# Kernel tuning notes

Hardware: AMD Instinct MI355X
Metric: run time of the kernel (lower is better)

The kernel has to match this reference:

```python
import jax, jax.numpy as jnp
import numpy as np

B, L = 8192, 2048  # L = 2*T, interleaved (dx, dy) increments


def setup_inputs() -> dict:
    key = jax.random.key(0)
    k1, k2, k3 = jax.random.split(key, 3)
    return {
        "traj_pred": jax.random.normal(k1, (B, L), dtype=jnp.float32),
        "traj_du_true": jax.random.normal(k2, (B, L), dtype=jnp.float32),  # unused in loss math
        "traj_pos_true": jax.random.normal(k3, (B, L), dtype=jnp.float32),
    }


def reference(traj_pred, traj_du_true, traj_pos_true):
    # pred[2k], pred[2k+1] are per-step (dx, dy) increments -> cumulative position
    T = traj_pred.shape[1] // 2
    d = traj_pred.reshape(traj_pred.shape[0], T, 2)  # [B, T, 2]
    pos = jnp.cumsum(d, axis=1)                      # [B, T, 2] running (x, y)
    tx = traj_pos_true[:, :T]                        # true x positions
    ty = traj_pos_true[:, T:]                        # true y positions
    err = (pos[..., 0] - tx) ** 2 + (pos[..., 1] - ty) ** 2
    return jnp.sum(err)
```

## Files before the change

### kernel.cpp

```cpp
#include <hip/hip_runtime.h>


constexpr int L_DIM = 2048;
constexpr int T_DIM = 1024;
constexpr int ROWS_PER_BLOCK = 4;
constexpr int NJ = 8;

__global__ __launch_bounds__(256, 4) void traj_loss_kernel(
    const float* __restrict__ pred,
    const float* __restrict__ pos_true,
    float* __restrict__ partials,
    int B)
{
    const int wid  = threadIdx.x >> 6;
    const int lane = threadIdx.x & 63;
    const int row  = blockIdx.x * ROWS_PER_BLOCK + wid;

    float acc = 0.0f;

    if (row < B) {
        const float4* p4  = reinterpret_cast<const float4*>(pred + (size_t)row * L_DIM);
        const float2* tX2 = reinterpret_cast<const float2*>(pos_true + (size_t)row * L_DIM);
        const float2* tY2 = reinterpret_cast<const float2*>(pos_true + (size_t)row * L_DIM + T_DIM);

        float4 v[NJ];
        float2 tx[NJ], ty[NJ];
#pragma unroll
        for (int j = 0; j < NJ; ++j) v[j]  = p4[j * 64 + lane];
#pragma unroll
        for (int j = 0; j < NJ; ++j) tx[j] = tX2[j * 64 + lane];
#pragma unroll
        for (int j = 0; j < NJ; ++j) ty[j] = tY2[j * 64 + lane];

        asm volatile("" ::: "memory");

        float ox[NJ], oy[NJ];
        float ix[NJ], iy[NJ];
#pragma unroll
        for (int j = 0; j < NJ; ++j) {
            ox[j] = v[j].x + v[j].z;
            oy[j] = v[j].y + v[j].w;
            ix[j] = ox[j];
            iy[j] = oy[j];
        }
#pragma unroll
        for (int d = 1; d < 64; d <<= 1) {
#pragma unroll
            for (int j = 0; j < NJ; ++j) {
                float ux = __shfl_up(ix[j], d);
                float uy = __shfl_up(iy[j], d);
                if (lane >= d) { ix[j] += ux; iy[j] += uy; }
            }
        }

        float cx = 0.0f, cy = 0.0f;
#pragma unroll
        for (int j = 0; j < NJ; ++j) {
            const float totx = __shfl(ix[j], 63);
            const float toty = __shfl(iy[j], 63);
            const float bx = cx + (ix[j] - ox[j]);
            const float by = cy + (iy[j] - oy[j]);

            const float px0 = bx  + v[j].x;
            const float px1 = px0 + v[j].z;
            const float py0 = by  + v[j].y;
            const float py1 = py0 + v[j].w;

            float e;
            e = px0 - tx[j].x; acc += e * e;
            e = px1 - tx[j].y; acc += e * e;
            e = py0 - ty[j].x; acc += e * e;
            e = py1 - ty[j].y; acc += e * e;

            cx += totx;
            cy += toty;
        }
    }

#pragma unroll
    for (int d = 32; d >= 1; d >>= 1) acc += __shfl_xor(acc, d);

    __shared__ float warp_sums[ROWS_PER_BLOCK];
    if (lane == 0) warp_sums[wid] = acc;
    __syncthreads();

    if (threadIdx.x == 0) {
        float s = 0.0f;
#pragma unroll
        for (int w = 0; w < ROWS_PER_BLOCK; ++w) s += warp_sums[w];
        partials[blockIdx.x] = s;
    }
}

__global__ __launch_bounds__(256) void reduce_kernel(
    const float* __restrict__ partials, float* __restrict__ out, int n)
{
    const int lane = threadIdx.x & 63;
    const int wid  = threadIdx.x >> 6;

    float s = 0.0f;
    for (int i = threadIdx.x; i < n; i += 256) s += partials[i];

#pragma unroll
    for (int d = 32; d >= 1; d >>= 1) s += __shfl_xor(s, d);

    __shared__ float ws[4];
    if (lane == 0) ws[wid] = s;
    __syncthreads();

    if (threadIdx.x == 0) out[0] = ws[0] + ws[1] + ws[2] + ws[3];
}

extern "C" void kernel_launch(void* const* d_in, const int* in_sizes, int n_in,
                              void* d_out, int out_size, void* d_ws, size_t ws_size,
                              hipStream_t stream) {
    const float* pred     = (const float*)d_in[0];
    const float* pos_true = (const float*)d_in[2];
    float* out      = (float*)d_out;
    float* partials = (float*)d_ws;

    const int B = in_sizes[0] / L_DIM;
    const int grid = (B + ROWS_PER_BLOCK - 1) / ROWS_PER_BLOCK;

    traj_loss_kernel<<<grid, 256, 0, stream>>>(pred, pos_true, partials, B);
    reduce_kernel<<<1, 256, 0, stream>>>(partials, out, grid);
}
```

Baseline: 28.57 us.

## Split each row across a full block with cross-wave scan carry

Each row is now processed by a 256-thread block instead of one 64-lane wave. Each wave scans its own 128 float4 chunk and the wave totals are combined through shared memory to form the carry. This cuts per-thread registers and raises the number of waves available to hide memory latency. In exchange it adds a block barrier per row and four times as many partials for the final reduction.

```diff
diff --git a/kernel.cpp b/kernel.cpp
--- a/kernel.cpp
+++ b/kernel.cpp
@@ -3,93 +3,73 @@
 
 constexpr int L_DIM = 2048;
 constexpr int T_DIM = 1024;
-constexpr int ROWS_PER_BLOCK = 4;
-constexpr int NJ = 8;
 
-__global__ __launch_bounds__(256, 4) void traj_loss_kernel(
+__global__ __launch_bounds__(256) void traj_loss_kernel(
     const float* __restrict__ pred,
     const float* __restrict__ pos_true,
     float* __restrict__ partials,
     int B)
 {
-    const int wid  = threadIdx.x >> 6;
+    const int w    = threadIdx.x >> 6;
     const int lane = threadIdx.x & 63;
-    const int row  = blockIdx.x * ROWS_PER_BLOCK + wid;
+    const int row  = blockIdx.x;
+
+    const float4* p4  = reinterpret_cast<const float4*>(pred + (size_t)row * L_DIM);
+    const float2* tX2 = reinterpret_cast<const float2*>(pos_true + (size_t)row * L_DIM);
+    const float2* tY2 = reinterpret_cast<const float2*>(pos_true + (size_t)row * L_DIM + T_DIM);
+
+    const int k0 = w * 128 + lane;
+    float4 v0 = p4[k0],        v1 = p4[k0 + 64];
+    float2 tx0 = tX2[k0],      tx1 = tX2[k0 + 64];
+    float2 ty0 = tY2[k0],      ty1 = tY2[k0 + 64];
+
+    const float ox0 = v0.x + v0.z, oy0 = v0.y + v0.w;
+    const float ox1 = v1.x + v1.z, oy1 = v1.y + v1.w;
+
+    float ix0 = ox0, ix1 = ox1, iy0 = oy0, iy1 = oy1;
+#pragma unroll
+    for (int d = 1; d < 64; d <<= 1) {
+        float a = __shfl_up(ix0, d);
+        float b = __shfl_up(ix1, d);
+        float c = __shfl_up(iy0, d);
+        float e = __shfl_up(iy1, d);
+        if (lane >= d) { ix0 += a; ix1 += b; iy0 += c; iy1 += e; }
+    }
+    const float t0x = __shfl(ix0, 63), t0y = __shfl(iy0, 63);
+    const float t1x = __shfl(ix1, 63), t1y = __shfl(iy1, 63);
+
+    __shared__ float wsum_x[4], wsum_y[4];
+    __shared__ float warp_acc[4];
+    if (lane == 0) { wsum_x[w] = t0x + t1x; wsum_y[w] = t0y + t1y; }
+    __syncthreads();
+    float cx = 0.0f, cy = 0.0f;
+#pragma unroll
+    for (int ww = 0; ww < 3; ++ww)
+        if (ww < w) { cx += wsum_x[ww]; cy += wsum_y[ww]; }
 
     float acc = 0.0f;
-
-    if (row < B) {
-        const float4* p4  = reinterpret_cast<const float4*>(pred + (size_t)row * L_DIM);
-        const float2* tX2 = reinterpret_cast<const float2*>(pos_true + (size_t)row * L_DIM);
-        const float2* tY2 = reinterpret_cast<const float2*>(pos_true + (size_t)row * L_DIM + T_DIM);
-
-        float4 v[NJ];
-        float2 tx[NJ], ty[NJ];
-#pragma unroll
-        for (int j = 0; j < NJ; ++j) v[j]  = p4[j * 64 + lane];
-#pragma unroll
-        for (int j = 0; j < NJ; ++j) tx[j] = tX2[j * 64 + lane];
-#pragma unroll
-        for (int j = 0; j < NJ; ++j) ty[j] = tY2[j * 64 + lane];
-
-        asm volatile("" ::: "memory");
-
-        float ox[NJ], oy[NJ];
-        float ix[NJ], iy[NJ];
-#pragma unroll
-        for (int j = 0; j < NJ; ++j) {
-            ox[j] = v[j].x + v[j].z;
-            oy[j] = v[j].y + v[j].w;
-            ix[j] = ox[j];
-            iy[j] = oy[j];
-        }
-#pragma unroll
-        for (int d = 1; d < 64; d <<= 1) {
-#pragma unroll
-            for (int j = 0; j < NJ; ++j) {
-                float ux = __shfl_up(ix[j], d);
-                float uy = __shfl_up(iy[j], d);
-                if (lane >= d) { ix[j] += ux; iy[j] += uy; }
-            }
-        }
-
-        float cx = 0.0f, cy = 0.0f;
-#pragma unroll
-        for (int j = 0; j < NJ; ++j) {
-            const float totx = __shfl(ix[j], 63);
-            const float toty = __shfl(iy[j], 63);
-            const float bx = cx + (ix[j] - ox[j]);
-            const float by = cy + (iy[j] - oy[j]);
-
-            const float px0 = bx  + v[j].x;
-            const float px1 = px0 + v[j].z;
-            const float py0 = by  + v[j].y;
-            const float py1 = py0 + v[j].w;
-
-            float e;
-            e = px0 - tx[j].x; acc += e * e;
-            e = px1 - tx[j].y; acc += e * e;
-            e = py0 - ty[j].x; acc += e * e;
-            e = py1 - ty[j].y; acc += e * e;
-
-            cx += totx;
-            cy += toty;
-        }
+    {
+        float rx = cx + (ix0 - ox0), ry = cy + (iy0 - oy0), e;
+        rx += v0.x; e = rx - tx0.x; acc += e * e;
+        ry += v0.y; e = ry - ty0.x; acc += e * e;
+        rx += v0.z; e = rx - tx0.y; acc += e * e;
+        ry += v0.w; e = ry - ty0.y; acc += e * e;
+    }
+    {
+        float rx = cx + t0x + (ix1 - ox1), ry = cy + t0y + (iy1 - oy1), e;
+        rx += v1.x; e = rx - tx1.x; acc += e * e;
+        ry += v1.y; e = ry - ty1.x; acc += e * e;
+        rx += v1.z; e = rx - tx1.y; acc += e * e;
+        ry += v1.w; e = ry - ty1.y; acc += e * e;
     }
 
 #pragma unroll
     for (int d = 32; d >= 1; d >>= 1) acc += __shfl_xor(acc, d);
 
-    __shared__ float warp_sums[ROWS_PER_BLOCK];
-    if (lane == 0) warp_sums[wid] = acc;
+    if (lane == 0) warp_acc[w] = acc;
     __syncthreads();
-
-    if (threadIdx.x == 0) {
-        float s = 0.0f;
-#pragma unroll
-        for (int w = 0; w < ROWS_PER_BLOCK; ++w) s += warp_sums[w];
-        partials[blockIdx.x] = s;
-    }
+    if (threadIdx.x == 0)
+        partials[row] = warp_acc[0] + warp_acc[1] + warp_acc[2] + warp_acc[3];
 }
 
 __global__ __launch_bounds__(256) void reduce_kernel(
@@ -120,8 +100,7 @@
     float* partials = (float*)d_ws;
 
     const int B = in_sizes[0] / L_DIM;
-    const int grid = (B + ROWS_PER_BLOCK - 1) / ROWS_PER_BLOCK;
 
-    traj_loss_kernel<<<grid, 256, 0, stream>>>(pred, pos_true, partials, B);
-    reduce_kernel<<<1, 256, 0, stream>>>(partials, out, grid);
+    traj_loss_kernel<<<B, 256, 0, stream>>>(pred, pos_true, partials, B);
+    reduce_kernel<<<1, 256, 0, stream>>>(partials, out, B);
 }
```

Result: slower. 35.18 us (+23.1%).
